# Optimization experiments

Measured on AMD Instinct MI355X. Metric: run time of the kernel, lower is better.

## Reference

```python
import jax, jax.numpy as jnp
import numpy as np

N_NODES = 100000
NEG_SLOPE = 0.2  # PyG GATConv default


def gat_conv(x, src, dst, W, a_src, a_dst, n_nodes):
    """One PyG-style GATConv (with self-loops already appended to src/dst).
    x: [N, Fin], W: [Fin, H*C], a_src/a_dst: [H, C]. Returns [N, H, C]."""
    H, C = a_src.shape
    h = (x @ W).reshape(-1, H, C)                      # [N, H, C]
    s_src = jnp.einsum('nhc,hc->nh', h, a_src)         # [N, H]
    s_dst = jnp.einsum('nhc,hc->nh', h, a_dst)         # [N, H]
    e = jax.nn.leaky_relu(s_src[src] + s_dst[dst], NEG_SLOPE)  # [E, H]
    # segment softmax over incoming edges of each destination node
    e_max = jax.ops.segment_max(e, dst, num_segments=n_nodes)  # [N, H]
    e_exp = jnp.exp(e - e_max[dst])
    denom = jax.ops.segment_sum(e_exp, dst, num_segments=n_nodes)
    alpha = e_exp / (denom[dst] + 1e-16)               # [E, H]
    msg = h[src] * alpha[:, :, None]                   # [E, H, C]
    return jax.ops.segment_sum(msg, dst, num_segments=n_nodes)  # [N, H, C]


def setup_inputs() -> dict:
    key = jax.random.key(0)
    ks = jax.random.split(key, 10)
    in_dim, hidden, heads, out_dim = 128, 32, 4, 32
    N, E = N_NODES, 1600000
    x = jax.random.normal(ks[0], (N, in_dim), dtype=jnp.float32)
    edge_index = jax.random.randint(ks[1], (2, E), 0, N, dtype=jnp.int64)
    s = 0.1
    return {
        'x': x,
        'edge_index': edge_index,
        'W1': s * jax.random.normal(ks[2], (in_dim, heads * hidden), dtype=jnp.float32),
        'a_src1': s * jax.random.normal(ks[3], (heads, hidden), dtype=jnp.float32),
        'a_dst1': s * jax.random.normal(ks[4], (heads, hidden), dtype=jnp.float32),
        'b1': jnp.zeros((heads * hidden,), dtype=jnp.float32),
        'W2': s * jax.random.normal(ks[5], (heads * hidden, out_dim), dtype=jnp.float32),
        'a_src2': s * jax.random.normal(ks[6], (1, out_dim), dtype=jnp.float32),
        'a_dst2': s * jax.random.normal(ks[7], (1, out_dim), dtype=jnp.float32),
        'b2': jnp.zeros((out_dim,), dtype=jnp.float32),
    }


def reference(x, edge_index, W1, a_src1, a_dst1, b1, W2, a_src2, a_dst2, b2):
    N = x.shape[0]
    loops = jnp.arange(N, dtype=edge_index.dtype)
    src = jnp.concatenate([edge_index[0], loops])  # PyG adds self-loops
    dst = jnp.concatenate([edge_index[1], loops])
    h1 = gat_conv(x, src, dst, W1, a_src1, a_dst1, N)      # [N, H, C]
    h1 = jax.nn.elu(h1.reshape(N, -1) + b1)                # concat heads + bias, elu
    h2 = gat_conv(h1, src, dst, W2, a_src2, a_dst2, N)     # [N, 1, out]
    return h2.mean(axis=1) + b2                            # concat=False -> mean over heads
```

## Files before the change

kernel.cpp:

```cpp
#include <hip/hip_runtime.h>
#include <hip/hip_bf16.h>

#define NEG 0.2f
#define BK_SHIFT 9
#define BK_CAP 9216

typedef short short8 __attribute__((ext_vector_type(8)));
typedef float f32x4 __attribute__((ext_vector_type(4)));

__device__ __forceinline__ float lrelu(float x){ return x > 0.f ? x : NEG * x; }
__device__ __forceinline__ float elu_f(float x){ return x > 0.f ? x : expm1f(x); }
__device__ __forceinline__ unsigned short f2bf(float f){
  unsigned int u = __float_as_uint(f);
  unsigned int r = u + 0x7fffu + ((u >> 16) & 1u);
  return (unsigned short)(r >> 16);
}
__device__ __forceinline__ float bf2f(unsigned short u){
  return __uint_as_float(((unsigned int)u) << 16);
}

__global__ __launch_bounds__(512) void k_binA(
    const int* __restrict__ src, const int* __restrict__ dst, int E,
    int* __restrict__ gcursor, int2* __restrict__ ebuf){
  __shared__ int hist[256];
  __shared__ int base[256];
  int t = threadIdx.x;
  if (t < 256) hist[t] = 0;
  __syncthreads();
  int e0 = blockIdx.x * 4096;
  for (int j = 0; j < 8; j++){
    int e = e0 + j * 512 + t;
    if (e < E) atomicAdd(&hist[dst[e] >> BK_SHIFT], 1);
  }
  __syncthreads();
  if (t < 256){
    int cnt = hist[t];
    if (cnt > 0) base[t] = atomicAdd(&gcursor[t], cnt);
    hist[t] = 0;
  }
  __syncthreads();
  for (int j = 0; j < 8; j++){
    int e = e0 + j * 512 + t;
    if (e < E){
      int d = dst[e]; int b = d >> BK_SHIFT;
      int loc = atomicAdd(&hist[b], 1);
      ebuf[(size_t)b * BK_CAP + base[b] + loc] = make_int2(src[e], d);
    }
  }
}

__global__ __launch_bounds__(1024) void k_csrC(
    const int2* __restrict__ ebuf, const int* __restrict__ gcount,
    int* __restrict__ rowp, int* __restrict__ csr, int N, int NBK, int total){
  __shared__ int hist[512];
  __shared__ int psum[256];
  __shared__ int bsum[256];
  int b = blockIdx.x, t = threadIdx.x;
  int nbase = b << BK_SHIFT;
  int cnt = gcount[b];
  const int2* eb = ebuf + (size_t)b * BK_CAP;
  if (t < 512) hist[t] = 0;
  int bv = 0;
  if (t < 256){
    int nodes = 0;
    if (t < NBK){ int nb = N - (t << BK_SHIFT); nodes = nb > 512 ? 512 : nb; bv = gcount[t] + nodes; }
    bsum[t] = bv;
  }
  __syncthreads();
  for (int off = 1; off < 256; off <<= 1){
    int x = (t >= off && t < 256) ? bsum[t - off] : 0;
    __syncthreads();
    if (t < 256) bsum[t] += x;
    __syncthreads();
  }
  for (int i = t; i < cnt; i += 1024)
    atomicAdd(&hist[eb[i].y - nbase], 1);
  __syncthreads();
  int v0 = 0, v1 = 0, ps = 0;
  if (t < 256){ v0 = hist[2 * t]; v1 = hist[2 * t + 1]; ps = v0 + v1; psum[t] = ps; }
  __syncthreads();
  for (int off = 1; off < 256; off <<= 1){
    int x = (t >= off && t < 256) ? psum[t - off] : 0;
    __syncthreads();
    if (t < 256) psum[t] += x;
    __syncthreads();
  }
  if (t < 256){
    int eo = psum[t] - ps;
    int bb = (b == 0) ? 0 : bsum[b - 1];
    int n0 = 2 * t, n1 = 2 * t + 1;
    int r0 = bb + eo + n0;
    int r1 = bb + eo + v0 + n1;
    if (nbase + n0 < N) rowp[nbase + n0] = r0;
    if (nbase + n1 < N) rowp[nbase + n1] = r1;
    hist[n0] = r0; hist[n1] = r1;
  }
  if (b == 0 && t == 0) rowp[N] = total;
  __syncthreads();
  for (int i = t; i < cnt; i += 1024){
    int2 e = eb[i];
    int pos = atomicAdd(&hist[e.y - nbase], 1);
    csr[pos] = e.x;
  }
  __syncthreads();
  if (t < 256){
    int n0 = 2 * t, n1 = 2 * t + 1;
    if (nbase + n0 < N) csr[hist[n0]] = nbase + n0;
    if (nbase + n1 < N) csr[hist[n1]] = nbase + n1;
  }
}

__global__ __launch_bounds__(128) void k_packW(
    const float* __restrict__ W, unsigned short* __restrict__ Wp){
  int n = blockIdx.x, k = threadIdx.x;
  Wp[n * 128 + k] = f2bf(W[(size_t)k * 128 + n]);
}

__global__ __launch_bounds__(256, 3) void k_gemm1(
    const float* __restrict__ x, const unsigned short* __restrict__ Wp,
    const float* __restrict__ a_src, const float* __restrict__ a_dst,
    unsigned short* __restrict__ h_bf, float* __restrict__ ss, float* __restrict__ sd, int N){
  __shared__ unsigned short Wt[128 * 136];
  __shared__ unsigned short Xb[64 * 136];
  int t = threadIdx.x;
  int rb = blockIdx.x * 64;

  #pragma unroll
  for (int j = 0; j < 8; j++){
    int fi = j * 256 + t;
    int n = fi >> 4, ch = fi & 15;
    *(uint4*)&Wt[n * 136 + ch * 8] = *(const uint4*)&Wp[n * 128 + ch * 8];
  }
  #pragma unroll
  for (int j = 0; j < 8; j++){
    int fi = j * 256 + t;
    int row = fi >> 5, k4 = (fi & 31) * 4;
    int gr = rb + row;
    float4 v = make_float4(0.f, 0.f, 0.f, 0.f);
    if (gr < N) v = *(const float4*)&x[(size_t)gr * 128 + k4];
    uint2 pk;
    pk.x = ((unsigned)f2bf(v.y) << 16) | f2bf(v.x);
    pk.y = ((unsigned)f2bf(v.w) << 16) | f2bf(v.z);
    *(uint2*)&Xb[row * 136 + k4] = pk;
  }
  __syncthreads();

  int w = t >> 6, l = t & 63;
  int m = l & 15, quad = l >> 4;
  f32x4 acc[8];
  #pragma unroll
  for (int ct = 0; ct < 8; ct++) acc[ct] = (f32x4){0.f, 0.f, 0.f, 0.f};

  #pragma unroll
  for (int kc = 0; kc < 4; kc++){
    short8 a = *(const short8*)&Xb[(w * 16 + m) * 136 + kc * 32 + quad * 8];
    #pragma unroll
    for (int ct = 0; ct < 8; ct++){
      short8 b = *(const short8*)&Wt[(ct * 16 + m) * 136 + kc * 32 + quad * 8];
      acc[ct] = __builtin_amdgcn_mfma_f32_16x16x32_bf16(a, b, acc[ct], 0, 0, 0);
    }
  }

  float as[8], ad[8];
  #pragma unroll
  for (int ct = 0; ct < 8; ct++){ as[ct] = a_src[ct * 16 + m]; ad[ct] = a_dst[ct * 16 + m]; }

  #pragma unroll
  for (int reg = 0; reg < 4; reg++){
    int gr = rb + w * 16 + quad * 4 + reg;
    bool ok = gr < N;
    if (ok){
      #pragma unroll
      for (int ct = 0; ct < 8; ct++)
        h_bf[(size_t)gr * 128 + ct * 16 + m] = f2bf(acc[ct][reg]);
    }
    #pragma unroll
    for (int hh = 0; hh < 4; hh++){
      float ps = acc[2*hh][reg] * as[2*hh] + acc[2*hh+1][reg] * as[2*hh+1];
      float pd = acc[2*hh][reg] * ad[2*hh] + acc[2*hh+1][reg] * ad[2*hh+1];
      ps += __shfl_xor(ps, 1, 16); ps += __shfl_xor(ps, 2, 16);
      ps += __shfl_xor(ps, 4, 16); ps += __shfl_xor(ps, 8, 16);
      pd += __shfl_xor(pd, 1, 16); pd += __shfl_xor(pd, 2, 16);
      pd += __shfl_xor(pd, 4, 16); pd += __shfl_xor(pd, 8, 16);
      if (m == 0 && ok){ ss[(size_t)gr * 4 + hh] = ps; sd[(size_t)gr * 4 + hh] = pd; }
    }
  }
}

__global__ __launch_bounds__(256) void k_agg1(
    const int* __restrict__ row_ptr, const int* __restrict__ csr_src,
    const float* __restrict__ ss, const float* __restrict__ sdst,
    const __hip_bfloat162* __restrict__ hb2,
    unsigned int* __restrict__ out1_bf, int N){
  int n = blockIdx.x * 4 + (threadIdx.x >> 6);
  if (n >= N) return;
  int l = threadIdx.x & 63;
  int hd = l >> 4;
  float sdv = sdst[(size_t)n * 4 + hd];
  int j8 = l & 7, hh8 = (l >> 3) & 3;
  float sw8 = sdst[(size_t)n * 4 + hh8];
  int j4 = l & 3, hh4 = (l >> 2) & 3;
  float sw4 = sdst[(size_t)n * 4 + hh4];
  int beg = row_ptr[n], end = row_ptr[n + 1];
  float ax = 0.f, ay = 0.f, sw = 0.f;
  int e = beg;
  for (; e + 8 <= end; e += 8){
    int sj = csr_src[e + j8];
    float wv = __expf(lrelu(ss[(size_t)sj * 4 + hh8] + sw8));
    int s0 = __shfl(sj, 0, 8), s1 = __shfl(sj, 1, 8), s2 = __shfl(sj, 2, 8), s3 = __shfl(sj, 3, 8);
    int s4 = __shfl(sj, 4, 8), s5 = __shfl(sj, 5, 8), s6 = __shfl(sj, 6, 8), s7 = __shfl(sj, 7, 8);
    float w0 = __shfl(wv, hd * 8 + 0, 32), w1 = __shfl(wv, hd * 8 + 1, 32);
    float w2 = __shfl(wv, hd * 8 + 2, 32), w3 = __shfl(wv, hd * 8 + 3, 32);
    float w4 = __shfl(wv, hd * 8 + 4, 32), w5 = __shfl(wv, hd * 8 + 5, 32);
    float w6 = __shfl(wv, hd * 8 + 6, 32), w7 = __shfl(wv, hd * 8 + 7, 32);
    float2 v0 = __bfloat1622float2(hb2[(size_t)s0 * 64 + l]);
    float2 v1 = __bfloat1622float2(hb2[(size_t)s1 * 64 + l]);
    float2 v2 = __bfloat1622float2(hb2[(size_t)s2 * 64 + l]);
    float2 v3 = __bfloat1622float2(hb2[(size_t)s3 * 64 + l]);
    float2 v4 = __bfloat1622float2(hb2[(size_t)s4 * 64 + l]);
    float2 v5 = __bfloat1622float2(hb2[(size_t)s5 * 64 + l]);
    float2 v6 = __bfloat1622float2(hb2[(size_t)s6 * 64 + l]);
    float2 v7 = __bfloat1622float2(hb2[(size_t)s7 * 64 + l]);
    ax += w0*v0.x + w1*v1.x + w2*v2.x + w3*v3.x + w4*v4.x + w5*v5.x + w6*v6.x + w7*v7.x;
    ay += w0*v0.y + w1*v1.y + w2*v2.y + w3*v3.y + w4*v4.y + w5*v5.y + w6*v6.y + w7*v7.y;
    sw += w0 + w1 + w2 + w3 + w4 + w5 + w6 + w7;
  }
  for (; e + 4 <= end; e += 4){
    int sj = csr_src[e + j4];
    float wv = __expf(lrelu(ss[(size_t)sj * 4 + hh4] + sw4));
    int s0 = __shfl(sj, 0, 4), s1 = __shfl(sj, 1, 4);
    int s2 = __shfl(sj, 2, 4), s3 = __shfl(sj, 3, 4);
    float w0 = __shfl(wv, hd * 4 + 0, 16), w1 = __shfl(wv, hd * 4 + 1, 16);
    float w2 = __shfl(wv, hd * 4 + 2, 16), w3 = __shfl(wv, hd * 4 + 3, 16);
    float2 v0 = __bfloat1622float2(hb2[(size_t)s0 * 64 + l]);
    float2 v1 = __bfloat1622float2(hb2[(size_t)s1 * 64 + l]);
    float2 v2 = __bfloat1622float2(hb2[(size_t)s2 * 64 + l]);
    float2 v3 = __bfloat1622float2(hb2[(size_t)s3 * 64 + l]);
    ax += w0*v0.x + w1*v1.x + w2*v2.x + w3*v3.x;
    ay += w0*v0.y + w1*v1.y + w2*v2.y + w3*v3.y;
    sw += w0 + w1 + w2 + w3;
  }
  for (; e < end; e++){
    int s = csr_src[e];
    float w = __expf(lrelu(ss[(size_t)s * 4 + hd] + sdv));
    float2 v = __bfloat1622float2(hb2[(size_t)s * 64 + l]);
    ax += w*v.x; ay += w*v.y; sw += w;
  }
  float inv = 1.f / (sw + 1e-16f);
  unsigned int lo = f2bf(ax * inv), hi = f2bf(ay * inv);
  out1_bf[(size_t)n * 64 + l] = (hi << 16) | lo;
}

__global__ __launch_bounds__(256) void k_gemm2(
    const unsigned int* __restrict__ out1_bf, const float* __restrict__ b1,
    const float* __restrict__ W2,
    const float* __restrict__ a_src, const float* __restrict__ a_dst,
    unsigned short* __restrict__ h2_bf, float* __restrict__ s_src2, float* __restrict__ s_dst2, int N){
  __shared__ __align__(16) float Wl[128 * 32];
  __shared__ __align__(16) float Xl[64 * 132];
  int t = threadIdx.x;
  int rb = blockIdx.x * 64;

  const float4* Wg4 = (const float4*)W2;
  float4* Wl4 = (float4*)Wl;
  #pragma unroll
  for (int j = 0; j < 4; j++) Wl4[j * 256 + t] = Wg4[j * 256 + t];

  #pragma unroll
  for (int j = 0; j < 4; j++){
    int fi = j * 256 + t;
    int row = fi >> 4, q = fi & 15;
    int gr = rb + row;
    float v[8] = {0.f,0.f,0.f,0.f,0.f,0.f,0.f,0.f};
    if (gr < N){
      uint4 u = *(const uint4*)&out1_bf[(size_t)gr * 64 + q * 4];
      float4 bva = *(const float4*)&b1[q * 8];
      float4 bvb = *(const float4*)&b1[q * 8 + 4];
      v[0] = elu_f(bf2f((unsigned short)(u.x & 0xffff)) + bva.x);
      v[1] = elu_f(bf2f((unsigned short)(u.x >> 16))    + bva.y);
      v[2] = elu_f(bf2f((unsigned short)(u.y & 0xffff)) + bva.z);
      v[3] = elu_f(bf2f((unsigned short)(u.y >> 16))    + bva.w);
      v[4] = elu_f(bf2f((unsigned short)(u.z & 0xffff)) + bvb.x);
      v[5] = elu_f(bf2f((unsigned short)(u.z >> 16))    + bvb.y);
      v[6] = elu_f(bf2f((unsigned short)(u.w & 0xffff)) + bvb.z);
      v[7] = elu_f(bf2f((unsigned short)(u.w >> 16))    + bvb.w);
    }
    #pragma unroll
    for (int i = 0; i < 8; i++) Xl[row * 132 + q * 8 + i] = v[i];
  }
  __syncthreads();

  int cg = t & 7, rg = t >> 3;
  int c0 = cg * 4, r0 = rg * 2;
  float acc[2][4] = {};

  #pragma unroll 8
  for (int k = 0; k < 128; k++){
    float a0 = Xl[r0 * 132 + k];
    float a1 = Xl[(r0 + 1) * 132 + k];
    float4 b = *(float4*)&Wl[k * 32 + c0];
    acc[0][0] += a0 * b.x; acc[0][1] += a0 * b.y; acc[0][2] += a0 * b.z; acc[0][3] += a0 * b.w;
    acc[1][0] += a1 * b.x; acc[1][1] += a1 * b.y; acc[1][2] += a1 * b.z; acc[1][3] += a1 * b.w;
  }

  float as[4], ad[4];
  #pragma unroll
  for (int j = 0; j < 4; j++){ as[j] = a_src[c0 + j]; ad[j] = a_dst[c0 + j]; }
  #pragma unroll
  for (int i = 0; i < 2; i++){
    int row = rb + r0 + i;
    if (row < N){
      ushort4 o;
      o.x = f2bf(acc[i][0]); o.y = f2bf(acc[i][1]); o.z = f2bf(acc[i][2]); o.w = f2bf(acc[i][3]);
      *(ushort4*)&h2_bf[(size_t)row * 32 + c0] = o;
    }
    float ps = 0.f, pd = 0.f;
    #pragma unroll
    for (int j = 0; j < 4; j++){ ps += acc[i][j] * as[j]; pd += acc[i][j] * ad[j]; }
    ps += __shfl_xor(ps, 1, 8); ps += __shfl_xor(ps, 2, 8); ps += __shfl_xor(ps, 4, 8);
    pd += __shfl_xor(pd, 1, 8); pd += __shfl_xor(pd, 2, 8); pd += __shfl_xor(pd, 4, 8);
    if ((t & 7) == 0 && row < N){ s_src2[row] = ps; s_dst2[row] = pd; }
  }
}

__global__ __launch_bounds__(256) void k_agg2(
    const int* __restrict__ row_ptr, const int* __restrict__ csr_src,
    const float* __restrict__ ss2, const float* __restrict__ sd2,
    const unsigned short* __restrict__ h2bf, const float* __restrict__ b2,
    float* __restrict__ out, int N){
  int n = blockIdx.x * 8 + (threadIdx.x >> 5);
  if (n >= N) return;
  int c = threadIdx.x & 31;
  float sdv = sd2[n];
  int beg = row_ptr[n], end = row_ptr[n + 1];
  float acc = 0.f, sw = 0.f;
  int e = beg;
  int j8 = c & 7;
  for (; e + 8 <= end; e += 8){
    int sj = csr_src[e + j8];
    float wv = __expf(lrelu(ss2[sj] + sdv));
    int s0 = __shfl(sj, 0, 8), s1 = __shfl(sj, 1, 8), s2 = __shfl(sj, 2, 8), s3 = __shfl(sj, 3, 8);
    int s4 = __shfl(sj, 4, 8), s5 = __shfl(sj, 5, 8), s6 = __shfl(sj, 6, 8), s7 = __shfl(sj, 7, 8);
    float w0 = __shfl(wv, 0, 8), w1 = __shfl(wv, 1, 8), w2 = __shfl(wv, 2, 8), w3 = __shfl(wv, 3, 8);
    float w4 = __shfl(wv, 4, 8), w5 = __shfl(wv, 5, 8), w6 = __shfl(wv, 6, 8), w7 = __shfl(wv, 7, 8);
    float v0 = bf2f(h2bf[(size_t)s0 * 32 + c]);
    float v1 = bf2f(h2bf[(size_t)s1 * 32 + c]);
    float v2 = bf2f(h2bf[(size_t)s2 * 32 + c]);
    float v3 = bf2f(h2bf[(size_t)s3 * 32 + c]);
    float v4 = bf2f(h2bf[(size_t)s4 * 32 + c]);
    float v5 = bf2f(h2bf[(size_t)s5 * 32 + c]);
    float v6 = bf2f(h2bf[(size_t)s6 * 32 + c]);
    float v7 = bf2f(h2bf[(size_t)s7 * 32 + c]);
    acc += w0*v0 + w1*v1 + w2*v2 + w3*v3 + w4*v4 + w5*v5 + w6*v6 + w7*v7;
    sw += w0 + w1 + w2 + w3 + w4 + w5 + w6 + w7;
  }
  for (; e + 4 <= end; e += 4){
    int s0 = csr_src[e], s1 = csr_src[e+1], s2 = csr_src[e+2], s3 = csr_src[e+3];
    int sj = csr_src[e + (c & 3)];
    float wv = __expf(lrelu(ss2[sj] + sdv));
    float w0 = __shfl(wv, 0, 4), w1 = __shfl(wv, 1, 4);
    float w2 = __shfl(wv, 2, 4), w3 = __shfl(wv, 3, 4);
    float v0 = bf2f(h2bf[(size_t)s0 * 32 + c]);
    float v1 = bf2f(h2bf[(size_t)s1 * 32 + c]);
    float v2 = bf2f(h2bf[(size_t)s2 * 32 + c]);
    float v3 = bf2f(h2bf[(size_t)s3 * 32 + c]);
    acc += w0*v0 + w1*v1 + w2*v2 + w3*v3;
    sw += w0 + w1 + w2 + w3;
  }
  for (; e < end; e++){
    int s = csr_src[e];
    float w = __expf(lrelu(ss2[s] + sdv));
    acc += w * bf2f(h2bf[(size_t)s * 32 + c]);
    sw += w;
  }
  out[(size_t)n * 32 + c] = acc / (sw + 1e-16f) + b2[c];
}

extern "C" void kernel_launch(void* const* d_in, const int* in_sizes, int n_in,
                              void* d_out, int out_size, void* d_ws, size_t ws_size,
                              hipStream_t stream) {
  const float* x      = (const float*)d_in[0];
  const int*   ei     = (const int*)  d_in[1];
  const float* W1     = (const float*)d_in[2];
  const float* a_src1 = (const float*)d_in[3];
  const float* a_dst1 = (const float*)d_in[4];
  const float* b1     = (const float*)d_in[5];
  const float* W2     = (const float*)d_in[6];
  const float* a_src2 = (const float*)d_in[7];
  const float* a_dst2 = (const float*)d_in[8];
  const float* b2     = (const float*)d_in[9];
  float* out = (float*)d_out;

  int N = in_sizes[0] / 128;
  int E = in_sizes[1] / 2;
  const int* srcp = ei;
  const int* dstp = ei + E;
  int total = E + N;
  int NBK = (N + 511) >> 9;

  char* p = (char*)d_ws;
  auto alloc = [&](size_t bytes) -> void* {
    void* r = (void*)p; p += (bytes + 255) & ~(size_t)255; return r;
  };
  unsigned short* h_bf    = (unsigned short*)alloc((size_t)N * 128 * 2);
  unsigned int*   out1_bf = (unsigned int*)alloc((size_t)N * 64 * 4);
  unsigned short* h2_bf   = (unsigned short*)alloc((size_t)N * 32 * 2);
  unsigned short* Wp      = (unsigned short*)alloc(128 * 128 * 2);
  float* ss1  = (float*)alloc((size_t)N * 4 * 4);
  float* sd1  = (float*)alloc((size_t)N * 4 * 4);
  float* ss2  = (float*)alloc((size_t)N * 4);
  float* sd2  = (float*)alloc((size_t)N * 4);
  int* rowp   = (int*)alloc((size_t)(N + 1) * 4);
  int* csr    = (int*)alloc((size_t)total * 4);
  int* gcur   = (int*)alloc(256 * 4);
  int2* ebuf  = (int2*)out1_bf;
  (void)ws_size; (void)n_in; (void)out_size;

  hipMemsetAsync(gcur, 0, 256 * 4, stream);
  k_binA<<<(E + 4095) / 4096, 512, 0, stream>>>(srcp, dstp, E, gcur, ebuf);
  k_csrC<<<NBK, 1024, 0, stream>>>(ebuf, gcur, rowp, csr, N, NBK, total);

  k_packW<<<128, 128, 0, stream>>>(W1, Wp);
  k_gemm1<<<(N + 63) / 64, 256, 0, stream>>>(x, Wp, a_src1, a_dst1, h_bf, ss1, sd1, N);
  k_agg1<<<(N + 3) / 4, 256, 0, stream>>>(rowp, csr, ss1, sd1, (const __hip_bfloat162*)h_bf, out1_bf, N);
  k_gemm2<<<(N + 63) / 64, 256, 0, stream>>>(out1_bf, b1, W2, a_src2, a_dst2, h2_bf, ss2, sd2, N);
  k_agg2<<<(N + 7) / 8, 256, 0, stream>>>(rowp, csr, ss2, sd2, h2_bf, b2, out, N);
}
```

Measured before the change: 310.4 us.

## Fold W packing into binning kernel, nontemporal edge stores, two-pass agg2 by source half

The W1 bf16 pack/transpose moves into an extra block of the edge-binning kernel, which removes one launch. Edge-buffer writes become packed 64-bit nontemporal stores. The layer-2 aggregation now scans each node's edge list twice, gathering sources below N/2 first and the rest second, so the gathered h2 rows stay in a smaller cache-resident window at any time. The trade is that every edge index is read twice, and the aggregation loses its 8-wide shuffle-based batching, which reduces memory-level parallelism.

```diff
diff --git a/kernel.cpp b/kernel.cpp
--- a/kernel.cpp
+++ b/kernel.cpp
@@ -21,10 +21,19 @@
 
 __global__ __launch_bounds__(512) void k_binA(
     const int* __restrict__ src, const int* __restrict__ dst, int E,
-    int* __restrict__ gcursor, int2* __restrict__ ebuf){
+    int* __restrict__ gcursor, int2* __restrict__ ebuf,
+    const float* __restrict__ W, unsigned short* __restrict__ Wp){
   __shared__ int hist[256];
   __shared__ int base[256];
   int t = threadIdx.x;
+  if (blockIdx.x == gridDim.x - 1){
+    for (int j = 0; j < 32; j++){
+      int idx = j * 512 + t;
+      int n = idx >> 7, k = idx & 127;
+      Wp[n * 128 + k] = f2bf(W[(size_t)k * 128 + n]);
+    }
+    return;
+  }
   if (t < 256) hist[t] = 0;
   __syncthreads();
   int e0 = blockIdx.x * 4096;
@@ -44,7 +53,9 @@
     if (e < E){
       int d = dst[e]; int b = d >> BK_SHIFT;
       int loc = atomicAdd(&hist[b], 1);
-      ebuf[(size_t)b * BK_CAP + base[b] + loc] = make_int2(src[e], d);
+      unsigned long long pk = ((unsigned long long)(unsigned)d << 32) | (unsigned)src[e];
+      __builtin_nontemporal_store(pk,
+        (unsigned long long*)&ebuf[(size_t)b * BK_CAP + base[b] + loc]);
     }
   }
 }
@@ -108,12 +119,6 @@
     if (nbase + n0 < N) csr[hist[n0]] = nbase + n0;
     if (nbase + n1 < N) csr[hist[n1]] = nbase + n1;
   }
-}
-
-__global__ __launch_bounds__(128) void k_packW(
-    const float* __restrict__ W, unsigned short* __restrict__ Wp){
-  int n = blockIdx.x, k = threadIdx.x;
-  Wp[n * 128 + k] = f2bf(W[(size_t)k * 128 + n]);
 }
 
 __global__ __launch_bounds__(256, 3) void k_gemm1(
@@ -327,51 +332,35 @@
     const int* __restrict__ row_ptr, const int* __restrict__ csr_src,
     const float* __restrict__ ss2, const float* __restrict__ sd2,
     const unsigned short* __restrict__ h2bf, const float* __restrict__ b2,
-    float* __restrict__ out, int N){
+    float* __restrict__ out, int N, int HALF){
   int n = blockIdx.x * 8 + (threadIdx.x >> 5);
   if (n >= N) return;
   int c = threadIdx.x & 31;
   float sdv = sd2[n];
   int beg = row_ptr[n], end = row_ptr[n + 1];
   float acc = 0.f, sw = 0.f;
-  int e = beg;
-  int j8 = c & 7;
-  for (; e + 8 <= end; e += 8){
-    int sj = csr_src[e + j8];
-    float wv = __expf(lrelu(ss2[sj] + sdv));
-    int s0 = __shfl(sj, 0, 8), s1 = __shfl(sj, 1, 8), s2 = __shfl(sj, 2, 8), s3 = __shfl(sj, 3, 8);
-    int s4 = __shfl(sj, 4, 8), s5 = __shfl(sj, 5, 8), s6 = __shfl(sj, 6, 8), s7 = __shfl(sj, 7, 8);
-    float w0 = __shfl(wv, 0, 8), w1 = __shfl(wv, 1, 8), w2 = __shfl(wv, 2, 8), w3 = __shfl(wv, 3, 8);
-    float w4 = __shfl(wv, 4, 8), w5 = __shfl(wv, 5, 8), w6 = __shfl(wv, 6, 8), w7 = __shfl(wv, 7, 8);
-    float v0 = bf2f(h2bf[(size_t)s0 * 32 + c]);
-    float v1 = bf2f(h2bf[(size_t)s1 * 32 + c]);
-    float v2 = bf2f(h2bf[(size_t)s2 * 32 + c]);
-    float v3 = bf2f(h2bf[(size_t)s3 * 32 + c]);
-    float v4 = bf2f(h2bf[(size_t)s4 * 32 + c]);
-    float v5 = bf2f(h2bf[(size_t)s5 * 32 + c]);
-    float v6 = bf2f(h2bf[(size_t)s6 * 32 + c]);
-    float v7 = bf2f(h2bf[(size_t)s7 * 32 + c]);
-    acc += w0*v0 + w1*v1 + w2*v2 + w3*v3 + w4*v4 + w5*v5 + w6*v6 + w7*v7;
-    sw += w0 + w1 + w2 + w3 + w4 + w5 + w6 + w7;
-  }
-  for (; e + 4 <= end; e += 4){
-    int s0 = csr_src[e], s1 = csr_src[e+1], s2 = csr_src[e+2], s3 = csr_src[e+3];
-    int sj = csr_src[e + (c & 3)];
-    float wv = __expf(lrelu(ss2[sj] + sdv));
-    float w0 = __shfl(wv, 0, 4), w1 = __shfl(wv, 1, 4);
-    float w2 = __shfl(wv, 2, 4), w3 = __shfl(wv, 3, 4);
-    float v0 = bf2f(h2bf[(size_t)s0 * 32 + c]);
-    float v1 = bf2f(h2bf[(size_t)s1 * 32 + c]);
-    float v2 = bf2f(h2bf[(size_t)s2 * 32 + c]);
-    float v3 = bf2f(h2bf[(size_t)s3 * 32 + c]);
-    acc += w0*v0 + w1*v1 + w2*v2 + w3*v3;
-    sw += w0 + w1 + w2 + w3;
-  }
-  for (; e < end; e++){
-    int s = csr_src[e];
-    float w = __expf(lrelu(ss2[s] + sdv));
-    acc += w * bf2f(h2bf[(size_t)s * 32 + c]);
-    sw += w;
+  #pragma unroll 1
+  for (int p = 0; p < 2; p++){
+    bool lowpass = (p == 0);
+    int e = beg;
+    for (; e + 2 <= end; e += 2){
+      int s0 = csr_src[e], s1 = csr_src[e + 1];
+      if ((s0 < HALF) == lowpass){
+        float w = __expf(lrelu(ss2[s0] + sdv));
+        acc += w * bf2f(h2bf[(size_t)s0 * 32 + c]); sw += w;
+      }
+      if ((s1 < HALF) == lowpass){
+        float w = __expf(lrelu(ss2[s1] + sdv));
+        acc += w * bf2f(h2bf[(size_t)s1 * 32 + c]); sw += w;
+      }
+    }
+    for (; e < end; e++){
+      int s = csr_src[e];
+      if ((s < HALF) == lowpass){
+        float w = __expf(lrelu(ss2[s] + sdv));
+        acc += w * bf2f(h2bf[(size_t)s * 32 + c]); sw += w;
+      }
+    }
   }
   out[(size_t)n * 32 + c] = acc / (sw + 1e-16f) + b2[c];
 }
@@ -417,12 +406,12 @@
   (void)ws_size; (void)n_in; (void)out_size;
 
   hipMemsetAsync(gcur, 0, 256 * 4, stream);
-  k_binA<<<(E + 4095) / 4096, 512, 0, stream>>>(srcp, dstp, E, gcur, ebuf);
+  int EB = (E + 4095) / 4096;
+  k_binA<<<EB + 1, 512, 0, stream>>>(srcp, dstp, E, gcur, ebuf, W1, Wp);
   k_csrC<<<NBK, 1024, 0, stream>>>(ebuf, gcur, rowp, csr, N, NBK, total);
 
-  k_packW<<<128, 128, 0, stream>>>(W1, Wp);
   k_gemm1<<<(N + 63) / 64, 256, 0, stream>>>(x, Wp, a_src1, a_dst1, h_bf, ss1, sd1, N);
   k_agg1<<<(N + 3) / 4, 256, 0, stream>>>(rowp, csr, ss1, sd1, (const __hip_bfloat162*)h_bf, out1_bf, N);
   k_gemm2<<<(N + 63) / 64, 256, 0, stream>>>(out1_bf, b1, W2, a_src2, a_dst2, h2_bf, ss2, sd2, N);
-  k_agg2<<<(N + 7) / 8, 256, 0, stream>>>(rowp, csr, ss2, sd2, h2_bf, b2, out, N);
-}
+  k_agg2<<<(N + 7) / 8, 256, 0, stream>>>(rowp, csr, ss2, sd2, h2_bf, b2, out, N, N / 2);
+}
```

After: 418.4 us. +34.8%, slower.
